# Optimization experiments

Measured on AMD Instinct MI355X. Metric: run time of the kernel, lower is better.

The kernel has to match this reference:

```python
import jax, jax.numpy as jnp
import numpy as np

B, T, IN, H, L = 64, 50, 256, 2000, 11  # L layers: 1 stem + 5 residual blocks of 2
EPS = 1e-4  # BatchNorm eps from module


def setup_inputs() -> dict:
    key = jax.random.key(0)
    ks = jax.random.split(key, 6)
    x = jax.random.normal(ks[0], (B, T, IN), jnp.float32)
    # InputMapping Linear weights, init uniform(-0.001, 0.001) per init_ih default
    W0 = jax.random.uniform(ks[1], (H, IN), jnp.float32, -0.001, 0.001)
    b0 = jnp.zeros((H,), jnp.float32)
    # recurrent diagonal weights, clipped to |u| <= hidden_max_abs=2
    u0 = jax.random.uniform(ks[2], (H,), jnp.float32, -1.0, 1.0)
    g0 = jnp.ones((H,), jnp.float32)   # BN gamma (shared across timesteps)
    be0 = jnp.zeros((H,), jnp.float32)  # BN beta
    Ws = jax.random.uniform(ks[3], (L - 1, H, H), jnp.float32, -0.001, 0.001)
    bs = jnp.zeros((L - 1, H), jnp.float32)
    us = jax.random.uniform(ks[4], (L - 1, H), jnp.float32, -1.0, 1.0)
    gs = jnp.ones((L - 1, H), jnp.float32)
    bes = jnp.zeros((L - 1, H), jnp.float32)
    return dict(x=x, W0=W0, b0=b0, u0=u0, g0=g0, be0=be0,
                Ws=Ws, bs=bs, us=us, gs=gs, bes=bes)


def _indrnn_layer(x, W, b, u, g, be):
    """InputMapping Linear -> per-timestep BatchNorm -> IndRNN scan (relu).
    x: (B,T,D) -> (B,T,H)"""
    m = jnp.einsum('btd,hd->bth', x, W) + b           # Linear per timestep
    mu = m.mean(axis=0, keepdims=True)                 # BN stats over batch, per (t, c)
    var = m.var(axis=0, keepdims=True)
    m = (m - mu) * jax.lax.rsqrt(var + EPS) * g + be

    def step(h, xt):
        h = jax.nn.relu(xt + u * h)                    # diagonal recurrence
        return h, h

    h0 = jnp.zeros((x.shape[0], u.shape[0]), x.dtype)
    _, hs = jax.lax.scan(step, h0, jnp.swapaxes(m, 0, 1))  # scan over time
    return jnp.swapaxes(hs, 0, 1)


def reference(x, W0, b0, u0, g0, be0, Ws, bs, us, gs, bes):
    # stem layer (input_size -> hidden)
    out = _indrnn_layer(x, W0, b0, u0, g0, be0)
    # residual blocks of residual_layers=2 with identity skip
    n = Ws.shape[0]  # 10
    i = 0
    while i < n:
        res = out
        out = _indrnn_layer(out, Ws[i], bs[i], us[i], gs[i], bes[i])
        if i + 1 < n:
            out = _indrnn_layer(out, Ws[i + 1], bs[i + 1], us[i + 1], gs[i + 1], bes[i + 1])
        out = out + res
        i += 2
    return out
```

## Files before the change

kernel.cpp:

```cpp
#include <hip/hip_runtime.h>

typedef unsigned short u16;
typedef __attribute__((ext_vector_type(8))) short bf16x8;
typedef __attribute__((ext_vector_type(4))) float f32x4;

#define NB 64
#define NT 50
#define NIN 256
#define NH 2000
#define HP 2048
#define EPS 1e-4f

__device__ __forceinline__ u16 f2bf(float f) {
  unsigned x = __float_as_uint(f);
  x += 0x7fffu + ((x >> 16) & 1u);
  return (u16)(x >> 16);
}
__device__ __forceinline__ float bf2f(u16 u) {
  return __uint_as_float(((unsigned)u) << 16);
}

#define GLDS16(g, l) __builtin_amdgcn_global_load_lds( \
  (const __attribute__((address_space(1))) unsigned int*)(g), \
  (__attribute__((address_space(3))) unsigned int*)(l), 16, 0, 0)

__global__ __launch_bounds__(256)
void cvt_all_kernel(const float* __restrict__ x, const float* __restrict__ W0,
                    const float* __restrict__ Ws, u16* __restrict__ x16,
                    u16* __restrict__ W016, u16* __restrict__ Ws16) {
  int bid = blockIdx.x;
  union { u16 u[8]; uint4 v; } o;
  if (bid < 400) {
    int tid = bid * 256 + threadIdx.x;
    int row = tid >> 5;
    int c8  = (tid & 31) << 3;
    int t = row >> 6, b = row & 63;
    const float* src = x + (size_t)(b * NT + t) * NIN + c8;
    float4 a = *(const float4*)src;
    float4 c = *(const float4*)(src + 4);
    o.u[0]=f2bf(a.x); o.u[1]=f2bf(a.y); o.u[2]=f2bf(a.z); o.u[3]=f2bf(a.w);
    o.u[4]=f2bf(c.x); o.u[5]=f2bf(c.y); o.u[6]=f2bf(c.z); o.u[7]=f2bf(c.w);
    *(uint4*)(x16 + (size_t)row * NIN + c8) = o.v;
  } else if (bid < 656) {
    int tid = (bid - 400) * 256 + threadIdx.x;
    int r = tid >> 5;
    int c8 = (tid & 31) << 3;
    if (r < NH) {
      const float* src = W0 + (size_t)r * NIN + c8;
      float4 a = *(const float4*)src;
      float4 b = *(const float4*)(src + 4);
      o.u[0]=f2bf(a.x); o.u[1]=f2bf(a.y); o.u[2]=f2bf(a.z); o.u[3]=f2bf(a.w);
      o.u[4]=f2bf(b.x); o.u[5]=f2bf(b.y); o.u[6]=f2bf(b.z); o.u[7]=f2bf(b.w);
    } else {
      o.v = make_uint4(0,0,0,0);
    }
    *(uint4*)(W016 + (size_t)tid * 8) = o.v;
  } else {
    int tid = (bid - 656) * 256 + threadIdx.x;
    int l  = tid >> 19;
    int r  = (tid >> 8) & 2047;
    int c8 = (tid & 255) << 3;
    if (r < NH && c8 < NH) {
      const float* src = Ws + (size_t)l * (NH * NH) + (size_t)r * NH + c8;
      float4 a = *(const float4*)src;
      float4 b = *(const float4*)(src + 4);
      o.u[0]=f2bf(a.x); o.u[1]=f2bf(a.y); o.u[2]=f2bf(a.z); o.u[3]=f2bf(a.w);
      o.u[4]=f2bf(b.x); o.u[5]=f2bf(b.y); o.u[6]=f2bf(b.z); o.u[7]=f2bf(b.w);
    } else {
      o.v = make_uint4(0,0,0,0);
    }
    *(uint4*)(Ws16 + (size_t)tid * 8) = o.v;
  }
}

__global__ __launch_bounds__(512, 4)
void gemm_bn_kernel(const u16* __restrict__ A, const u16* __restrict__ W,
                    u16* __restrict__ Mn, const float* __restrict__ g,
                    const float* __restrict__ be, int K) {
  __shared__ u16 As[4 * 128 * 32];
  __shared__ u16 Bs[4 * 128 * 32];
  const int tid = threadIdx.x;
  const int w = tid >> 6, l = tid & 63;
  const int wm = w >> 2, wn = w & 3;
  const int bid = blockIdx.x;
  const int xcd = bid & 7;
  const int r0  = bid >> 3;
  const int hi  = r0 >= 25;
  const int bn  = xcd + (hi << 3);
  const int bm  = r0 - 25 * hi;
  f32x4 acc[4][2] = {};
  const u16* Ab = A + (size_t)bm * 128 * K;
  const u16* Wb = W + (size_t)bn * 128 * K;

  const int srow = l >> 2;
  const int scb  = (l & 3) ^ (srow & 3);
  const size_t goff = (size_t)(w * 16 + srow) * K + scb * 8;
  const int lr  = l & 15;
  const int lkb = l >> 4;
  const int nk  = K >> 5;

#define STAGE(tt, bi) do {                                        \
    GLDS16(Ab + goff + (tt) * 32, As + (bi) * 4096 + w * 512);    \
    GLDS16(Wb + goff + (tt) * 32, Bs + (bi) * 4096 + w * 512);    \
  } while (0)

  STAGE(0, 0);
  STAGE(1, 1);
  STAGE(2, 2);
  asm volatile("s_waitcnt vmcnt(4)" ::: "memory");
  __builtin_amdgcn_s_barrier();

  for (int t = 0; t < nk; ++t) {
    if (t > 0) {
      int rem = nk - 1 - t;
      if (rem >= 2)      asm volatile("s_waitcnt vmcnt(4)" ::: "memory");
      else if (rem == 1) asm volatile("s_waitcnt vmcnt(2)" ::: "memory");
      else               asm volatile("s_waitcnt vmcnt(0)" ::: "memory");
      __builtin_amdgcn_s_barrier();
    }
    if (t + 3 < nk) {
      STAGE(t + 3, (t + 3) & 3);
    }
    const u16* Ac = As + (t & 3) * 4096;
    const u16* Bc = Bs + (t & 3) * 4096;
    bf16x8 af[4], bfr[2];
    const int cb = (lkb ^ (lr & 3)) * 8;
#pragma unroll
    for (int i = 0; i < 4; ++i)
      af[i] = *(const bf16x8*)(Ac + (wm * 64 + i * 16 + lr) * 32 + cb);
#pragma unroll
    for (int j = 0; j < 2; ++j)
      bfr[j] = *(const bf16x8*)(Bc + (wn * 32 + j * 16 + lr) * 32 + cb);
    __builtin_amdgcn_s_setprio(1);
#pragma unroll
    for (int i = 0; i < 4; ++i)
#pragma unroll
      for (int j = 0; j < 2; ++j)
        acc[i][j] = __builtin_amdgcn_mfma_f32_16x16x32_bf16(af[i], bfr[j], acc[i][j], 0, 0, 0);
    __builtin_amdgcn_s_setprio(0);
  }
#undef STAGE

  const int lg = l >> 4;
  const int rbase = bm * 128 + wm * 64;
  const int cbase = bn * 128 + wn * 32;
#pragma unroll
  for (int j = 0; j < 2; ++j) {
    float s = 0.f, s2 = 0.f;
#pragma unroll
    for (int i = 0; i < 4; ++i)
#pragma unroll
      for (int r = 0; r < 4; ++r) { float v = acc[i][j][r]; s += v; s2 += v * v; }
    s  += __shfl_xor(s, 16);  s2 += __shfl_xor(s2, 16);
    s  += __shfl_xor(s, 32);  s2 += __shfl_xor(s2, 32);
    float mu  = s * (1.f / 64.f);
    float var = fmaxf(s2 * (1.f / 64.f) - mu * mu, 0.f);
    int col = cbase + j * 16 + lr;
    bool ok = col < NH;
    float gg = ok ? g[col]  : 0.f;
    float bb = ok ? be[col] : 0.f;
    float sc = rsqrtf(var + EPS) * gg;
#pragma unroll
    for (int i = 0; i < 4; ++i) {
      int row0 = rbase + i * 16 + lg * 4;
#pragma unroll
      for (int r = 0; r < 4; ++r)
        Mn[(size_t)(row0 + r) * HP + col] = f2bf((acc[i][j][r] - mu) * sc + bb);
    }
  }
}

__device__ __forceinline__ void pad16(u16* out16, int b, int h) {
#pragma unroll
  for (int t = 0; t < NT; ++t)
    *(unsigned*)(out16 + (size_t)(t * NB + b) * HP + h) = 0u;
}

__global__ void scan_a_kernel(const u16* __restrict__ Mn, const float* __restrict__ u,
                              u16* __restrict__ out16) {
  int tid = blockIdx.x * 256 + threadIdx.x;
  int h2 = tid & 1023, b = tid >> 10;
  int h = h2 << 1;
  if (h >= NH) { pad16(out16, b, h); return; }
  unsigned mv[NT];
#pragma unroll
  for (int t = 0; t < NT; ++t)
    mv[t] = *(const unsigned*)(Mn + (size_t)(t * NB + b) * HP + h);
  float2 uu = *(const float2*)(u + h);
  float h0 = 0.f, h1 = 0.f;
#pragma unroll
  for (int t = 0; t < NT; ++t) {
    h0 = fmaxf(fmaf(uu.x, h0, bf2f((u16)(mv[t] & 0xffffu))), 0.f);
    h1 = fmaxf(fmaf(uu.y, h1, bf2f((u16)(mv[t] >> 16))), 0.f);
    *(unsigned*)(out16 + (size_t)(t * NB + b) * HP + h) =
        (unsigned)f2bf(h0) | ((unsigned)f2bf(h1) << 16);
  }
}

template<bool HASRES>
__global__ void scan_b_kernel(const u16* __restrict__ Mn, const float* __restrict__ u,
                              const u16* __restrict__ res16, u16* __restrict__ out16) {
  int tid = blockIdx.x * 256 + threadIdx.x;
  int h2 = tid & 1023, b = tid >> 10;
  int h = h2 << 1;
  if (h >= NH) { pad16(out16, b, h); return; }
  unsigned mv[NT];
#pragma unroll
  for (int t = 0; t < NT; ++t)
    mv[t] = *(const unsigned*)(Mn + (size_t)(t * NB + b) * HP + h);
  unsigned rv[NT];
  if (HASRES) {
#pragma unroll
    for (int t = 0; t < NT; ++t)
      rv[t] = *(const unsigned*)(res16 + (size_t)(t * NB + b) * HP + h);
  }
  float2 uu = *(const float2*)(u + h);
  float h0 = 0.f, h1 = 0.f;
#pragma unroll
  for (int t = 0; t < NT; ++t) {
    h0 = fmaxf(fmaf(uu.x, h0, bf2f((u16)(mv[t] & 0xffffu))), 0.f);
    h1 = fmaxf(fmaf(uu.y, h1, bf2f((u16)(mv[t] >> 16))), 0.f);
    float o0 = h0, o1 = h1;
    if (HASRES) {
      o0 += bf2f((u16)(rv[t] & 0xffffu));
      o1 += bf2f((u16)(rv[t] >> 16));
    }
    *(unsigned*)(out16 + (size_t)(t * NB + b) * HP + h) =
        (unsigned)f2bf(o0) | ((unsigned)f2bf(o1) << 16);
  }
}

__global__ void scan_c_kernel(const u16* __restrict__ Mn, const float* __restrict__ u,
                              const u16* __restrict__ res16, float* __restrict__ out) {
  int tid = blockIdx.x * 256 + threadIdx.x;
  int h2 = tid & 1023, b = tid >> 10;
  int h = h2 << 1;
  if (h >= NH) return;
  unsigned mv[NT];
#pragma unroll
  for (int t = 0; t < NT; ++t)
    mv[t] = *(const unsigned*)(Mn + (size_t)(t * NB + b) * HP + h);
  unsigned rv[NT];
#pragma unroll
  for (int t = 0; t < NT; ++t)
    rv[t] = *(const unsigned*)(res16 + (size_t)(t * NB + b) * HP + h);
  float2 uu = *(const float2*)(u + h);
  float h0 = 0.f, h1 = 0.f;
#pragma unroll
  for (int t = 0; t < NT; ++t) {
    h0 = fmaxf(fmaf(uu.x, h0, bf2f((u16)(mv[t] & 0xffffu))), 0.f);
    h1 = fmaxf(fmaf(uu.y, h1, bf2f((u16)(mv[t] >> 16))), 0.f);
    *(float2*)(out + (size_t)(b * NT + t) * NH + h) =
        make_float2(h0 + bf2f((u16)(rv[t] & 0xffffu)),
                    h1 + bf2f((u16)(rv[t] >> 16)));
  }
}

extern "C" void kernel_launch(void* const* d_in, const int* in_sizes, int n_in,
                              void* d_out, int out_size, void* d_ws, size_t ws_size,
                              hipStream_t stream) {
  const float* x   = (const float*)d_in[0];
  const float* W0  = (const float*)d_in[1];
  const float* u0  = (const float*)d_in[3];
  const float* g0  = (const float*)d_in[4];
  const float* be0 = (const float*)d_in[5];
  const float* Ws  = (const float*)d_in[6];
  const float* us  = (const float*)d_in[8];
  const float* gs  = (const float*)d_in[9];
  const float* bes = (const float*)d_in[10];
  float* out = (float*)d_out;

  char* ws = (char*)d_ws;
  u16*   x16  = (u16*)  (ws + 0);
  u16*   W016 = (u16*)  (ws + 1638400);
  u16*   Ws16 = (u16*)  (ws + 2686976);
  u16*   Mbuf = (u16*)  (ws + 86573056);
  u16*   A16  = (u16*)  (ws + 99680256);
  u16*   B16  = (u16*)  (ws + 112787456);

  cvt_all_kernel<<<21136, 256, 0, stream>>>(x, W0, Ws, x16, W016, Ws16);

  gemm_bn_kernel<<<400, 512, 0, stream>>>(x16, W016, Mbuf, g0, be0, NIN);
  scan_b_kernel<false><<<256, 256, 0, stream>>>(Mbuf, u0, nullptr, A16);

  for (int l = 0; l < 10; ++l) {
    const u16* Ain = (l & 1) ? B16 : A16;
    gemm_bn_kernel<<<400, 512, 0, stream>>>(Ain, Ws16 + (size_t)l * HP * HP, Mbuf,
                                            gs + (size_t)l * NH, bes + (size_t)l * NH, HP);
    const float* ul = us + (size_t)l * NH;
    if ((l & 1) == 0) {
      scan_a_kernel<<<256, 256, 0, stream>>>(Mbuf, ul, B16);
    } else if (l < 9) {
      scan_b_kernel<true><<<256, 256, 0, stream>>>(Mbuf, ul, A16, A16);
    } else {
      scan_c_kernel<<<256, 256, 0, stream>>>(Mbuf, ul, A16, out);
    }
  }
}
```

Before: 598.2 us.

## Switch GEMM K-loop to BK=64 double-buffered LDS pipeline

The GEMM+BN kernel now stages 64-wide K tiles with two LDS buffers instead of 32-wide K tiles with a 4-deep, 3-ahead prefetch ring. The swizzle changes to an 8-way XOR, and each iteration runs two 32-wide MFMA sub-steps. This halves the number of barriers per K range, but prefetch depth drops to one tile ahead, so latency hiding may be weaker. LDS use stays the same.

Result: faster. 504.3 us (median of 3 runs) (-15.7%).

```diff
diff --git a/kernel.cpp b/kernel.cpp
--- a/kernel.cpp
+++ b/kernel.cpp
@@ -77,8 +77,8 @@
 void gemm_bn_kernel(const u16* __restrict__ A, const u16* __restrict__ W,
                     u16* __restrict__ Mn, const float* __restrict__ g,
                     const float* __restrict__ be, int K) {
-  __shared__ u16 As[4 * 128 * 32];
-  __shared__ u16 Bs[4 * 128 * 32];
+  __shared__ u16 As[2 * 128 * 64];
+  __shared__ u16 Bs[2 * 128 * 64];
   const int tid = threadIdx.x;
   const int w = tid >> 6, l = tid & 63;
   const int wm = w >> 2, wn = w & 3;
@@ -92,52 +92,51 @@
   const u16* Ab = A + (size_t)bm * 128 * K;
   const u16* Wb = W + (size_t)bn * 128 * K;
 
-  const int srow = l >> 2;
-  const int scb  = (l & 3) ^ (srow & 3);
-  const size_t goff = (size_t)(w * 16 + srow) * K + scb * 8;
+  const int rib  = l >> 3;
+  const int scbs = (l & 7) ^ rib;
+  const size_t goff1 = (size_t)((2 * w    ) * 8 + rib) * K + scbs * 8;
+  const size_t goff2 = (size_t)((2 * w + 1) * 8 + rib) * K + scbs * 8;
   const int lr  = l & 15;
   const int lkb = l >> 4;
-  const int nk  = K >> 5;
-
-#define STAGE(tt, bi) do {                                        \
-    GLDS16(Ab + goff + (tt) * 32, As + (bi) * 4096 + w * 512);    \
-    GLDS16(Wb + goff + (tt) * 32, Bs + (bi) * 4096 + w * 512);    \
+  const int nk  = K >> 6;
+
+#define STAGE(tt, bi) do {                                              \
+    GLDS16(Ab + goff1 + (tt) * 64, As + (bi) * 8192 + (2*w    ) * 512); \
+    GLDS16(Ab + goff2 + (tt) * 64, As + (bi) * 8192 + (2*w + 1) * 512); \
+    GLDS16(Wb + goff1 + (tt) * 64, Bs + (bi) * 8192 + (2*w    ) * 512); \
+    GLDS16(Wb + goff2 + (tt) * 64, Bs + (bi) * 8192 + (2*w + 1) * 512); \
   } while (0)
 
   STAGE(0, 0);
-  STAGE(1, 1);
-  STAGE(2, 2);
-  asm volatile("s_waitcnt vmcnt(4)" ::: "memory");
+  asm volatile("s_waitcnt vmcnt(0)" ::: "memory");
   __builtin_amdgcn_s_barrier();
 
+  int p = 0;
   for (int t = 0; t < nk; ++t) {
-    if (t > 0) {
-      int rem = nk - 1 - t;
-      if (rem >= 2)      asm volatile("s_waitcnt vmcnt(4)" ::: "memory");
-      else if (rem == 1) asm volatile("s_waitcnt vmcnt(2)" ::: "memory");
-      else               asm volatile("s_waitcnt vmcnt(0)" ::: "memory");
-      __builtin_amdgcn_s_barrier();
-    }
-    if (t + 3 < nk) {
-      STAGE(t + 3, (t + 3) & 3);
-    }
-    const u16* Ac = As + (t & 3) * 4096;
-    const u16* Bc = Bs + (t & 3) * 4096;
-    bf16x8 af[4], bfr[2];
-    const int cb = (lkb ^ (lr & 3)) * 8;
-#pragma unroll
-    for (int i = 0; i < 4; ++i)
-      af[i] = *(const bf16x8*)(Ac + (wm * 64 + i * 16 + lr) * 32 + cb);
-#pragma unroll
-    for (int j = 0; j < 2; ++j)
-      bfr[j] = *(const bf16x8*)(Bc + (wn * 32 + j * 16 + lr) * 32 + cb);
-    __builtin_amdgcn_s_setprio(1);
-#pragma unroll
-    for (int i = 0; i < 4; ++i)
+    if (t + 1 < nk) STAGE(t + 1, p ^ 1);
+    const u16* Ac = As + p * 8192;
+    const u16* Bc = Bs + p * 8192;
+#pragma unroll
+    for (int kk = 0; kk < 2; ++kk) {
+      bf16x8 af[4], bfr[2];
+      const int cb = ((kk * 4 + lkb) ^ (lr & 7)) * 8;
+#pragma unroll
+      for (int i = 0; i < 4; ++i)
+        af[i] = *(const bf16x8*)(Ac + (wm * 64 + i * 16 + lr) * 64 + cb);
 #pragma unroll
       for (int j = 0; j < 2; ++j)
-        acc[i][j] = __builtin_amdgcn_mfma_f32_16x16x32_bf16(af[i], bfr[j], acc[i][j], 0, 0, 0);
-    __builtin_amdgcn_s_setprio(0);
+        bfr[j] = *(const bf16x8*)(Bc + (wn * 32 + j * 16 + lr) * 64 + cb);
+      __builtin_amdgcn_s_setprio(1);
+#pragma unroll
+      for (int i = 0; i < 4; ++i)
+#pragma unroll
+        for (int j = 0; j < 2; ++j)
+          acc[i][j] = __builtin_amdgcn_mfma_f32_16x16x32_bf16(af[i], bfr[j], acc[i][j], 0, 0, 0);
+      __builtin_amdgcn_s_setprio(0);
+    }
+    asm volatile("s_waitcnt vmcnt(0)" ::: "memory");
+    __builtin_amdgcn_s_barrier();
+    p ^= 1;
   }
 #undef STAGE
 
```
